# Kernel optimization log

Measured on AMD Instinct MI355X. Metric: run time of the kernel, lower is better.

Reference implementation:

```python
import jax, jax.numpy as jnp
import numpy as np

NUM_EMBEDDINGS = 1024
EMBEDDING_DIM = 64
COMMITMENT_COST = 0.25
DECAY = 0.99
EPS = 1e-5


def setup_inputs() -> dict:
    key = jax.random.key(0)
    k1, k2, k3 = jax.random.split(key, 3)
    z = jax.random.normal(k1, (64, EMBEDDING_DIM, 32, 32), dtype=jnp.float32)
    embedding = jax.random.normal(k2, (NUM_EMBEDDINGS, EMBEDDING_DIM), dtype=jnp.float32)
    cluster_size = jnp.zeros((NUM_EMBEDDINGS,), dtype=jnp.float32)
    ema_w = jax.random.normal(k3, (NUM_EMBEDDINGS, EMBEDDING_DIM), dtype=jnp.float32)
    return {"z": z, "embedding": embedding, "cluster_size": cluster_size, "ema_w": ema_w}


def reference(z, embedding, cluster_size, ema_w):
    B, D, H, W = z.shape
    K = embedding.shape[0]
    # (B, H, W, D) -> (N, D)
    z_flat = jnp.transpose(z, (0, 2, 3, 1)).reshape(-1, D)
    # squared L2 distances to every code: (N, K)
    d = (jnp.sum(z_flat * z_flat, axis=1, keepdims=True)
         + jnp.sum(embedding * embedding, axis=1)
         - 2.0 * z_flat @ embedding.T)
    indices = jnp.argmin(d, axis=1)  # (N,)
    z_q = embedding[indices].reshape(B, H, W, D).transpose(0, 3, 1, 2)

    # EMA codebook update (training branch); no gradients flow here in torch (.data ops)
    zf = jax.lax.stop_gradient(z_flat)
    counts = jax.ops.segment_sum(jnp.ones_like(zf[:, 0]), indices, num_segments=K)
    dw = jax.ops.segment_sum(zf, indices, num_segments=K)  # encodings.T @ z_flat
    new_cluster_size = DECAY * cluster_size + (1.0 - DECAY) * counts
    new_ema_w = DECAY * ema_w + (1.0 - DECAY) * dw
    n = jnp.sum(new_cluster_size)
    cs = (new_cluster_size + EPS) / (n + K * EPS) * n
    new_embedding = new_ema_w / cs[:, None]

    loss = COMMITMENT_COST * jnp.mean((z - jax.lax.stop_gradient(z_q)) ** 2)
    z_q_st = z + jax.lax.stop_gradient(z_q - z)  # straight-through
    return (z_q_st, loss, indices.reshape(B, H, W), new_cluster_size, new_ema_w, new_embedding)
```

## Files before the change

kernel.cpp:

```cpp
#include <hip/hip_runtime.h>
#include <stdint.h>

typedef unsigned short ushort;
typedef __attribute__((ext_vector_type(8)))  short bfrag;
typedef __attribute__((ext_vector_type(16))) float f32x16;

#define D      64
#define K      1024
#define HW     1024
#define NROWS  65536
#define NELEM  (NROWS * D)
#define BAND   0.01f

#define O_ZQ   0
#define O_LOSS 4194304
#define O_IDX  4194305
#define O_NCS  4259841
#define O_EMAW 4260865
#define O_EMB  4326401

#define WB_KEYS   0x000000
#define WB_BUCKET 0x040000
#define WB_EH     0x080000
#define WB_EL     0x0A0000
#define WB_ESQ    0x0C0000
#define WB_OFFS   0x0C1000
#define WB_CURSOR 0x0C2000
#define WB_COUNTS 0x0C3000
#define WB_LOSSN  0x0C4000
#define WB_RLIST  0x0C5000
#define WB_ZH     0x105000
#define WB_END_T1 0x905000

__device__ __forceinline__ unsigned bf16r(float x) {
    unsigned u = __float_as_uint(x);
    return (u + 0x7FFFu + ((u >> 16) & 1u)) >> 16;
}
__device__ __forceinline__ float bf16f(unsigned h) {
    return __uint_as_float(h << 16);
}

__global__ __launch_bounds__(64) void vq_prep_e(
    const float* __restrict__ emb, ushort* __restrict__ eh,
    ushort* __restrict__ el, float* __restrict__ esq)
{
    const int k = blockIdx.x * 64 + threadIdx.x;
    const float* er = emb + (size_t)k * 64;
    float a = 0.f;
    for (int d = 0; d < 64; ++d) {
        float v = er[d];
        a = fmaf(v, v, a);
        unsigned hh = bf16r(v);
        float rem = v - bf16f(hh);
        unsigned ll = bf16r(rem);
        eh[k * 64 + d] = (ushort)hh;
        el[k * 64 + d] = (ushort)ll;
    }
    esq[k] = a;
}

__global__ __launch_bounds__(256, 3) void vq_dist_kernel(
    const float* __restrict__ z, const short* __restrict__ eh_g,
    const short* __restrict__ el_g, const float* __restrict__ esq_g,
    int* __restrict__ keys, unsigned* __restrict__ counts,
    unsigned* __restrict__ rcnt, int* __restrict__ rlist,
    ushort* __restrict__ zh_g, int dump)
{
    __shared__ __align__(16) short zh_lds[128 * 64];
    __shared__ __align__(16) short zl_lds[128 * 64];
    __shared__ __align__(16) short eh_lds[64 * 64];
    __shared__ __align__(16) short el_lds[64 * 64];
    __shared__ float esq_lds[1024];

    const int tid  = threadIdx.x;
    const int lane = tid & 63;
    const int wave = tid >> 6;
    const int col  = lane & 31;
    const int h    = lane >> 5;
    const int n0   = blockIdx.x * 128;
    const int b    = n0 >> 10;
    const int hw0  = n0 & 1023;

    for (int it = 0; it < 4; ++it) {
        int task = it * 256 + tid;
        int row  = task & 127;
        int kq   = task >> 7;
        const float* zp = z + (size_t)b * 65536 + (size_t)(kq * 8) * 1024 + hw0 + row;
        bfrag vh, vl;
#pragma unroll
        for (int m = 0; m < 8; ++m) {
            float v = zp[m * 1024];
            unsigned hh = bf16r(v);
            float rem = v - bf16f(hh);
            vh[m] = (short)hh;
            vl[m] = (short)bf16r(rem);
        }
        int unit = kq ^ (row & 7);
        *(bfrag*)&zh_lds[row * 64 + unit * 8] = vh;
        *(bfrag*)&zl_lds[row * 64 + unit * 8] = vl;
    }
    for (int it = 0; it < 4; ++it) {
        int t = it * 256 + tid;
        esq_lds[t] = esq_g[t];
    }
    __syncthreads();

    const int wrow = wave * 32 + col;
    bfrag zhA[4], zlA[4];
#pragma unroll
    for (int j = 0; j < 4; ++j) {
        int kq = j * 2 + h;
        int unit = kq ^ (wrow & 7);
        zhA[j] = *(const bfrag*)&zh_lds[wrow * 64 + unit * 8];
        zlA[j] = *(const bfrag*)&zl_lds[wrow * 64 + unit * 8];
    }

    if (dump) {
        for (int it = 0; it < 4; ++it) {
            int task = it * 256 + tid;
            int row  = task >> 3;
            int kq   = task & 7;
            int unit = kq ^ (row & 7);
            uint4 v = *(const uint4*)&zh_lds[row * 64 + unit * 8];
            *(uint4*)&zh_g[(size_t)(n0 + row) * 64 + kq * 8] = v;
        }
    }

    float t1s[16], t2s[16];
    unsigned t1c[16];
#pragma unroll
    for (int i = 0; i < 16; ++i) { t1s[i] = INFINITY; t2s[i] = INFINITY; t1c[i] = 0; }

    bfrag pfh[2], pfl[2];
    auto loadE = [&](int cb) {
#pragma unroll
        for (int q = 0; q < 2; ++q) {
            int u = q * 256 + tid;
            int code = u >> 3, m = u & 7;
            pfh[q] = *(const bfrag*)&eh_g[(size_t)(cb + code) * 64 + m * 8];
            pfl[q] = *(const bfrag*)&el_g[(size_t)(cb + code) * 64 + m * 8];
        }
    };
    auto writeE = [&]() {
#pragma unroll
        for (int q = 0; q < 2; ++q) {
            int u = q * 256 + tid;
            int code = u >> 3, m = u & 7;
            int unit = ((code >> 5) * 4 + (m >> 1)) * 64 +
                       ((((m & 1) << 5) | (code & 31)) ^ (m & 7));
            *(bfrag*)&eh_lds[unit * 8] = pfh[q];
            *(bfrag*)&el_lds[unit * 8] = pfl[q];
        }
    };

    loadE(0);
    for (int ch = 0; ch < 16; ++ch) {
        const int cb = ch * 64;
        __syncthreads();
        writeE();
        __syncthreads();
        if (ch < 15) loadE(cb + 64);

#pragma unroll
        for (int t = 0; t < 2; ++t) {
            bfrag ehB[4], elB[4];
#pragma unroll
            for (int j = 0; j < 4; ++j) {
                int m = j * 2 + h;
                int unit = (t * 4 + j) * 64 + (((h << 5) | col) ^ (m & 7));
                ehB[j] = *(const bfrag*)&eh_lds[unit * 8];
                elB[j] = *(const bfrag*)&el_lds[unit * 8];
            }
            f32x16 acc1 = {}, acc2 = {};
#pragma unroll
            for (int j = 0; j < 4; ++j)
                acc1 = __builtin_amdgcn_mfma_f32_32x32x16_bf16(zhA[j], ehB[j], acc1, 0, 0, 0);
#pragma unroll
            for (int j = 0; j < 4; ++j)
                acc2 = __builtin_amdgcn_mfma_f32_32x32x16_bf16(zhA[j], elB[j], acc2, 0, 0, 0);
#pragma unroll
            for (int j = 0; j < 4; ++j)
                acc2 = __builtin_amdgcn_mfma_f32_32x32x16_bf16(zlA[j], ehB[j], acc2, 0, 0, 0);

            const float esqv = esq_lds[cb + t * 32 + col];
            const unsigned ccode = cb + t * 32 + col;
#pragma unroll
            for (int i = 0; i < 16; ++i) {
                float s = fmaf(-2.f, acc1[i], esqv);
                s = fmaf(-2.f, acc2[i], s);
                float mx = fmaxf(s, t1s[i]);
                t2s[i] = fminf(t2s[i], mx);
                bool lt = s < t1s[i];
                t1s[i] = fminf(t1s[i], s);
                t1c[i] = lt ? ccode : t1c[i];
            }
        }
    }

#pragma unroll
    for (int i = 0; i < 16; ++i) {
        float v = t1s[i], w = t2s[i];
        int   c = (int)t1c[i];
#pragma unroll
        for (int m = 1; m < 32; m <<= 1) {
            float ov = __shfl_xor(v, m);
            int   oc = __shfl_xor(c, m);
            float ow = __shfl_xor(w, m);
            float mx = fmaxf(v, ov);
            w = fminf(fminf(w, ow), mx);
            bool take = (ov < v) || (ov == v && oc < c);
            v = take ? ov : v;
            c = take ? oc : c;
        }
        if ((lane & 31) == 0) {
            int row = (i & 3) + ((i >> 2) << 3) + (h << 2);
            int n = n0 + wave * 32 + row;
            keys[n] = c;
            atomicAdd(&counts[c], 1u);
            if (w - v < BAND) {
                unsigned p = atomicAdd(rcnt, 1u);
                rlist[p] = n;
            }
        }
    }
}

__global__ __launch_bounds__(256) void vq_rescore(
    const float* __restrict__ z, const float* __restrict__ emb,
    const float* __restrict__ esq, const unsigned* __restrict__ rcnt,
    const int* __restrict__ rlist, int* __restrict__ keys,
    unsigned* __restrict__ counts)
{
    __shared__ float zrow[64];
    __shared__ float rs[4];
    __shared__ int   rc[4];
    const int tid = threadIdx.x;
    const unsigned cnt = rcnt[0];

    for (unsigned i = blockIdx.x; i < cnt; i += gridDim.x) {
        const int n = rlist[i];
        const int b = n >> 10, hw = n & 1023;
        __syncthreads();
        if (tid < 64) zrow[tid] = z[(size_t)b * 65536 + (size_t)tid * 1024 + hw];
        __syncthreads();

        float best = INFINITY; int bc = 0;
        for (int rep = 0; rep < 4; ++rep) {
            int code = rep * 256 + tid;
            const float4* er = (const float4*)(emb + (size_t)code * 64);
            float a0 = 0.f, a1 = 0.f, a2 = 0.f, a3 = 0.f;
#pragma unroll
            for (int q = 0; q < 16; ++q) {
                float4 e = er[q];
                a0 = fmaf(zrow[q * 4 + 0], e.x, a0);
                a1 = fmaf(zrow[q * 4 + 1], e.y, a1);
                a2 = fmaf(zrow[q * 4 + 2], e.z, a2);
                a3 = fmaf(zrow[q * 4 + 3], e.w, a3);
            }
            float s = fmaf(-2.f, (a0 + a1) + (a2 + a3), esq[code]);
            if (s < best || (s == best && code < bc)) { best = s; bc = code; }
        }
        for (int m = 1; m < 64; m <<= 1) {
            float ov = __shfl_xor(best, m);
            int   oc = __shfl_xor(bc, m);
            bool take = (ov < best) || (ov == best && oc < bc);
            best = take ? ov : best;
            bc   = take ? oc : bc;
        }
        if ((tid & 63) == 0) { rs[tid >> 6] = best; rc[tid >> 6] = bc; }
        __syncthreads();
        if (tid == 0) {
            float fb = rs[0]; int fc = rc[0];
#pragma unroll
            for (int q = 1; q < 4; ++q) {
                bool take = (rs[q] < fb) || (rs[q] == fb && rc[q] < fc);
                fb = take ? rs[q] : fb;
                fc = take ? rc[q] : fc;
            }
            int old = keys[n];
            if (fc != old) {
                atomicAdd(&counts[old], (unsigned)-1);
                atomicAdd(&counts[fc], 1u);
                keys[n] = fc;
            }
        }
    }
}

__global__ __launch_bounds__(1024) void vq_scan_kernel(
    const unsigned* __restrict__ counts, const float* __restrict__ cs,
    unsigned* __restrict__ offs, unsigned* __restrict__ cursor,
    float* __restrict__ out, float* __restrict__ n_val)
{
    __shared__ unsigned wtot[16], wbase[16];
    __shared__ float    fred[16];
    const int k    = threadIdx.x;
    const int lane = k & 63;
    const int w    = k >> 6;

    unsigned c = counts[k];
    unsigned v = c;
#pragma unroll
    for (int off = 1; off < 64; off <<= 1) {
        unsigned t = __shfl_up(v, off);
        if (lane >= off) v += t;
    }
    if (lane == 63) wtot[w] = v;

    float ncs = 0.99f * cs[k] + 0.01f * (float)c;
    out[O_NCS + k] = ncs;
    float s = ncs;
#pragma unroll
    for (int off = 32; off; off >>= 1) s += __shfl_down(s, off);
    if (lane == 0) fred[w] = s;

    __syncthreads();
    if (k == 0) {
        unsigned base = 0;
        float nt = 0.f;
#pragma unroll
        for (int i = 0; i < 16; ++i) {
            wbase[i] = base;
            base += wtot[i];
            nt += fred[i];
        }
        n_val[0] = nt;
    }
    __syncthreads();
    unsigned o = wbase[w] + (v - c);
    offs[k]   = o;
    cursor[k] = o;
}

__global__ __launch_bounds__(256) void vq_epilogue_kernel(
    const float* __restrict__ z, const float* __restrict__ emb,
    const int* __restrict__ keys, float* __restrict__ out,
    unsigned* __restrict__ cursor, int* __restrict__ bucket,
    float* __restrict__ loss_acc)
{
    const int tid = threadIdx.x;
    const int n   = blockIdx.x * 128 + (tid & 127);
    const int h   = tid >> 7;
    const int b   = n >> 10;
    const int hw  = n & 1023;
    const int k   = keys[n];

    const float*  zb  = z   + ((size_t)(b * D + h * 32)) * HW + hw;
    float*        oq  = out + O_ZQ + ((size_t)(b * D + h * 32)) * HW + hw;
    const float4* ek4 = (const float4*)emb + (size_t)k * 16 + h * 8;

    float lacc = 0.f;
#pragma unroll
    for (int i = 0; i < 8; ++i) {
        float4 e = ek4[i];
        float z0 = zb[(i * 4 + 0) * HW];
        float z1 = zb[(i * 4 + 1) * HW];
        float z2 = zb[(i * 4 + 2) * HW];
        float z3 = zb[(i * 4 + 3) * HW];
        oq[(i * 4 + 0) * HW] = z0 + (e.x - z0);
        oq[(i * 4 + 1) * HW] = z1 + (e.y - z1);
        oq[(i * 4 + 2) * HW] = z2 + (e.z - z2);
        oq[(i * 4 + 3) * HW] = z3 + (e.w - z3);
        float d0 = z0 - e.x, d1 = z1 - e.y, d2 = z2 - e.z, d3 = z3 - e.w;
        lacc = fmaf(d0, d0, lacc);
        lacc = fmaf(d1, d1, lacc);
        lacc = fmaf(d2, d2, lacc);
        lacc = fmaf(d3, d3, lacc);
    }

    if (h == 0) {
        out[O_IDX + n] = (float)k;
        unsigned pos = atomicAdd(&cursor[k], 1u);
        bucket[pos]  = n;
    }

    for (int off = 32; off; off >>= 1) lacc += __shfl_down(lacc, off);
    if ((tid & 63) == 0) atomicAdd(loss_acc, lacc);
}

template <int MODE>
__global__ __launch_bounds__(256) void vq_upd_kernel(
    const float* __restrict__ z, const ushort* __restrict__ zh,
    const int* __restrict__ bucket, const unsigned* __restrict__ offs,
    const unsigned* __restrict__ counts, const float* __restrict__ ema_w,
    const float* __restrict__ n_val, const float* __restrict__ loss_acc,
    float* __restrict__ out)
{
    __shared__ float red[4][64];
    const int k   = blockIdx.x;
    const int tid = threadIdx.x;
    const int d   = tid & 63;
    const int q   = tid >> 6;
    const unsigned off = offs[k];
    const unsigned cnt = counts[k];

    auto zload = [&](int r) -> float {
        if (MODE == 1)
            return __uint_as_float((unsigned)zh[(size_t)r * 64 + d] << 16);
        return z[(size_t)(r >> 10) * (D * HW) + (size_t)d * HW + (r & 1023)];
    };

    float acc = 0.f;
    unsigned j = q;
    for (; j + 12 < cnt; j += 16) {
        int r0 = bucket[off + j];
        int r1 = bucket[off + j + 4];
        int r2 = bucket[off + j + 8];
        int r3 = bucket[off + j + 12];
        acc += zload(r0); acc += zload(r1); acc += zload(r2); acc += zload(r3);
    }
    for (; j < cnt; j += 4) acc += zload(bucket[off + j]);

    red[q][d] = acc;
    __syncthreads();
    if (q == 0) {
        float dw = red[0][d] + red[1][d] + red[2][d] + red[3][d];
        float nw = 0.99f * ema_w[k * 64 + d] + 0.01f * dw;
        out[O_EMAW + k * 64 + d] = nw;
        float n   = n_val[0];
        float ncs = out[O_NCS + k];
        float csv = (ncs + 1e-5f) / (n + 1024e-5f) * n;
        out[O_EMB + k * 64 + d] = nw / csv;
    }
    if (k == 0 && tid == 0)
        out[O_LOSS] = 0.25f * loss_acc[0] / (float)NELEM;
}

extern "C" void kernel_launch(void* const* d_in, const int* in_sizes, int n_in,
                              void* d_out, int out_size, void* d_ws, size_t ws_size,
                              hipStream_t stream) {
    const float* z     = (const float*)d_in[0];
    const float* emb   = (const float*)d_in[1];
    const float* cs    = (const float*)d_in[2];
    const float* ema_w = (const float*)d_in[3];
    float* out = (float*)d_out;

    char* W = (char*)d_ws;
    int*      keys   = (int*)(W + WB_KEYS);
    int*      bucket = (int*)(W + WB_BUCKET);
    short*    eh_g   = (short*)(W + WB_EH);
    short*    el_g   = (short*)(W + WB_EL);
    float*    esq    = (float*)(W + WB_ESQ);
    unsigned* offs   = (unsigned*)(W + WB_OFFS);
    unsigned* cursor = (unsigned*)(W + WB_CURSOR);
    unsigned* counts = (unsigned*)(W + WB_COUNTS);
    float*    lossa  = (float*)(W + WB_LOSSN);
    float*    n_val  = lossa + 1;
    unsigned* rcnt   = (unsigned*)(W + WB_LOSSN + 8);
    int*      rlist  = (int*)(W + WB_RLIST);
    ushort*   zh_g   = (ushort*)(W + WB_ZH);

    const int dump = ws_size >= (size_t)WB_END_T1 ? 1 : 0;

    hipMemsetAsync(W + WB_COUNTS, 0, 0x2000, stream);

    vq_prep_e<<<16, 64, 0, stream>>>(emb, (ushort*)eh_g, (ushort*)el_g, esq);
    vq_dist_kernel<<<512, 256, 0, stream>>>(z, eh_g, el_g, esq, keys, counts,
                                            rcnt, rlist, zh_g, dump);
    vq_rescore<<<96, 256, 0, stream>>>(z, emb, esq, rcnt, rlist, keys, counts);
    vq_scan_kernel<<<1, 1024, 0, stream>>>(counts, cs, offs, cursor, out, n_val);
    vq_epilogue_kernel<<<512, 256, 0, stream>>>(z, emb, keys, out, cursor,
                                                bucket, lossa);
    if (dump)
        vq_upd_kernel<1><<<1024, 256, 0, stream>>>(z, zh_g, bucket, offs, counts,
                                                   ema_w, n_val, lossa, out);
    else
        vq_upd_kernel<0><<<1024, 256, 0, stream>>>(z, zh_g, bucket, offs, counts,
                                                   ema_w, n_val, lossa, out);
}
```

Before: 251.1 us.

## Restructure VQ pipeline: double-buffered codebook, fused distance MFMA, scatter z rows via output

The distance kernel now double-buffers codebook chunks in LDS, so each chunk needs one barrier instead of two. It pre-scales z by -2 and seeds the accumulator with the squared code norms, so a single MFMA accumulator gives the distance and the second-best tracking becomes one fmed3. Indices go straight into the output buffer instead of a keys array. The epilogue is split in two: a scatter kernel writes z rows in fp32 row-major into the z_q output region, bucketed by code, and the update kernel reads them contiguously. A final kernel then overwrites that region with the real z_q. The codebook prep kernel is parallelised per element, and the rescore grid is enlarged. Together this removes the bf16 z dump and the indirect bucket gathers, in exchange for an extra full pass over z and using the output region as scratch.

```diff
diff --git a/kernel.cpp b/kernel.cpp
--- a/kernel.cpp
+++ b/kernel.cpp
@@ -19,18 +19,14 @@
 #define O_EMAW 4260865
 #define O_EMB  4326401
 
-#define WB_KEYS   0x000000
-#define WB_BUCKET 0x040000
-#define WB_EH     0x080000
-#define WB_EL     0x0A0000
-#define WB_ESQ    0x0C0000
-#define WB_OFFS   0x0C1000
-#define WB_CURSOR 0x0C2000
-#define WB_COUNTS 0x0C3000
-#define WB_LOSSN  0x0C4000
-#define WB_RLIST  0x0C5000
-#define WB_ZH     0x105000
-#define WB_END_T1 0x905000
+#define WB_EH     0x00000
+#define WB_EL     0x20000
+#define WB_ESQ    0x40000
+#define WB_OFFS   0x41000
+#define WB_CURSOR 0x42000
+#define WB_COUNTS 0x43000
+#define WB_LOSSN  0x44000
+#define WB_RLIST  0x45000
 
 __device__ __forceinline__ unsigned bf16r(float x) {
     unsigned u = __float_as_uint(x);
@@ -44,32 +40,29 @@
     const float* __restrict__ emb, ushort* __restrict__ eh,
     ushort* __restrict__ el, float* __restrict__ esq)
 {
-    const int k = blockIdx.x * 64 + threadIdx.x;
-    const float* er = emb + (size_t)k * 64;
-    float a = 0.f;
-    for (int d = 0; d < 64; ++d) {
-        float v = er[d];
-        a = fmaf(v, v, a);
-        unsigned hh = bf16r(v);
-        float rem = v - bf16f(hh);
-        unsigned ll = bf16r(rem);
-        eh[k * 64 + d] = (ushort)hh;
-        el[k * 64 + d] = (ushort)ll;
-    }
-    esq[k] = a;
-}
-
-__global__ __launch_bounds__(256, 3) void vq_dist_kernel(
+    const int k = blockIdx.x;
+    const int d = threadIdx.x;
+    float v = emb[k * 64 + d];
+    unsigned hh = bf16r(v);
+    float rem = v - bf16f(hh);
+    eh[k * 64 + d] = (ushort)hh;
+    el[k * 64 + d] = (ushort)bf16r(rem);
+    float a = v * v;
+#pragma unroll
+    for (int off = 32; off; off >>= 1) a += __shfl_xor(a, off);
+    if (d == 0) esq[k] = a;
+}
+
+__global__ __launch_bounds__(256, 2) void vq_dist_kernel(
     const float* __restrict__ z, const short* __restrict__ eh_g,
     const short* __restrict__ el_g, const float* __restrict__ esq_g,
-    int* __restrict__ keys, unsigned* __restrict__ counts,
-    unsigned* __restrict__ rcnt, int* __restrict__ rlist,
-    ushort* __restrict__ zh_g, int dump)
+    float* __restrict__ out, unsigned* __restrict__ counts,
+    unsigned* __restrict__ rcnt, int* __restrict__ rlist)
 {
     __shared__ __align__(16) short zh_lds[128 * 64];
     __shared__ __align__(16) short zl_lds[128 * 64];
-    __shared__ __align__(16) short eh_lds[64 * 64];
-    __shared__ __align__(16) short el_lds[64 * 64];
+    __shared__ __align__(16) short eh_lds[2][64 * 64];
+    __shared__ __align__(16) short el_lds[2][64 * 64];
     __shared__ float esq_lds[1024];
 
     const int tid  = threadIdx.x;
@@ -89,9 +82,9 @@
         bfrag vh, vl;
 #pragma unroll
         for (int m = 0; m < 8; ++m) {
-            float v = zp[m * 1024];
-            unsigned hh = bf16r(v);
-            float rem = v - bf16f(hh);
+            float t = -2.0f * zp[m * 1024];
+            unsigned hh = bf16r(t);
+            float rem = t - bf16f(hh);
             vh[m] = (short)hh;
             vl[m] = (short)bf16r(rem);
         }
@@ -103,6 +96,32 @@
         int t = it * 256 + tid;
         esq_lds[t] = esq_g[t];
     }
+
+    bfrag pfh[2], pfl[2];
+    auto loadE = [&](int cb) {
+#pragma unroll
+        for (int q = 0; q < 2; ++q) {
+            int u = q * 256 + tid;
+            int code = u >> 3, m = u & 7;
+            pfh[q] = *(const bfrag*)&eh_g[(size_t)(cb + code) * 64 + m * 8];
+            pfl[q] = *(const bfrag*)&el_g[(size_t)(cb + code) * 64 + m * 8];
+        }
+    };
+    auto writeE = [&](int buf) {
+#pragma unroll
+        for (int q = 0; q < 2; ++q) {
+            int u = q * 256 + tid;
+            int code = u >> 3, m = u & 7;
+            int unit = ((code >> 5) * 4 + (m >> 1)) * 64 +
+                       ((((m & 1) << 5) | (code & 31)) ^ (m & 7));
+            *(bfrag*)&eh_lds[buf][unit * 8] = pfh[q];
+            *(bfrag*)&el_lds[buf][unit * 8] = pfl[q];
+        }
+    };
+
+    loadE(0);
+    writeE(0);
+    loadE(64);
     __syncthreads();
 
     const int wrow = wave * 32 + col;
@@ -115,86 +134,55 @@
         zlA[j] = *(const bfrag*)&zl_lds[wrow * 64 + unit * 8];
     }
 
-    if (dump) {
-        for (int it = 0; it < 4; ++it) {
-            int task = it * 256 + tid;
-            int row  = task >> 3;
-            int kq   = task & 7;
-            int unit = kq ^ (row & 7);
-            uint4 v = *(const uint4*)&zh_lds[row * 64 + unit * 8];
-            *(uint4*)&zh_g[(size_t)(n0 + row) * 64 + kq * 8] = v;
-        }
-    }
-
     float t1s[16], t2s[16];
     unsigned t1c[16];
 #pragma unroll
     for (int i = 0; i < 16; ++i) { t1s[i] = INFINITY; t2s[i] = INFINITY; t1c[i] = 0; }
 
-    bfrag pfh[2], pfl[2];
-    auto loadE = [&](int cb) {
-#pragma unroll
-        for (int q = 0; q < 2; ++q) {
-            int u = q * 256 + tid;
-            int code = u >> 3, m = u & 7;
-            pfh[q] = *(const bfrag*)&eh_g[(size_t)(cb + code) * 64 + m * 8];
-            pfl[q] = *(const bfrag*)&el_g[(size_t)(cb + code) * 64 + m * 8];
-        }
-    };
-    auto writeE = [&]() {
-#pragma unroll
-        for (int q = 0; q < 2; ++q) {
-            int u = q * 256 + tid;
-            int code = u >> 3, m = u & 7;
-            int unit = ((code >> 5) * 4 + (m >> 1)) * 64 +
-                       ((((m & 1) << 5) | (code & 31)) ^ (m & 7));
-            *(bfrag*)&eh_lds[unit * 8] = pfh[q];
-            *(bfrag*)&el_lds[unit * 8] = pfl[q];
-        }
-    };
-
-    loadE(0);
     for (int ch = 0; ch < 16; ++ch) {
-        const int cb = ch * 64;
-        __syncthreads();
-        writeE();
-        __syncthreads();
-        if (ch < 15) loadE(cb + 64);
+        const int cb  = ch * 64;
+        const int buf = ch & 1;
 
 #pragma unroll
         for (int t = 0; t < 2; ++t) {
+            const int ccode = cb + t * 32 + col;
+            const float esqv = esq_lds[ccode];
             bfrag ehB[4], elB[4];
 #pragma unroll
             for (int j = 0; j < 4; ++j) {
                 int m = j * 2 + h;
                 int unit = (t * 4 + j) * 64 + (((h << 5) | col) ^ (m & 7));
-                ehB[j] = *(const bfrag*)&eh_lds[unit * 8];
-                elB[j] = *(const bfrag*)&el_lds[unit * 8];
-            }
-            f32x16 acc1 = {}, acc2 = {};
+                ehB[j] = *(const bfrag*)&eh_lds[buf][unit * 8];
+                elB[j] = *(const bfrag*)&el_lds[buf][unit * 8];
+            }
+            f32x16 acc;
+#pragma unroll
+            for (int i = 0; i < 16; ++i) acc[i] = esqv;
 #pragma unroll
             for (int j = 0; j < 4; ++j)
-                acc1 = __builtin_amdgcn_mfma_f32_32x32x16_bf16(zhA[j], ehB[j], acc1, 0, 0, 0);
+                acc = __builtin_amdgcn_mfma_f32_32x32x16_bf16(zhA[j], ehB[j], acc, 0, 0, 0);
 #pragma unroll
             for (int j = 0; j < 4; ++j)
-                acc2 = __builtin_amdgcn_mfma_f32_32x32x16_bf16(zhA[j], elB[j], acc2, 0, 0, 0);
+                acc = __builtin_amdgcn_mfma_f32_32x32x16_bf16(zhA[j], elB[j], acc, 0, 0, 0);
 #pragma unroll
             for (int j = 0; j < 4; ++j)
-                acc2 = __builtin_amdgcn_mfma_f32_32x32x16_bf16(zlA[j], ehB[j], acc2, 0, 0, 0);
-
-            const float esqv = esq_lds[cb + t * 32 + col];
-            const unsigned ccode = cb + t * 32 + col;
+                acc = __builtin_amdgcn_mfma_f32_32x32x16_bf16(zlA[j], ehB[j], acc, 0, 0, 0);
+
 #pragma unroll
             for (int i = 0; i < 16; ++i) {
-                float s = fmaf(-2.f, acc1[i], esqv);
-                s = fmaf(-2.f, acc2[i], s);
-                float mx = fmaxf(s, t1s[i]);
-                t2s[i] = fminf(t2s[i], mx);
+                float s = acc[i];
+                t2s[i] = __builtin_amdgcn_fmed3f(t1s[i], t2s[i], s);
                 bool lt = s < t1s[i];
                 t1s[i] = fminf(t1s[i], s);
-                t1c[i] = lt ? ccode : t1c[i];
-            }
-        }
+                t1c[i] = lt ? (unsigned)ccode : t1c[i];
+            }
+        }
+
+        if (ch < 15) {
+            writeE(buf ^ 1);
+            if (ch < 14) loadE(cb + 128);
+        }
+        __syncthreads();
     }
 
 #pragma unroll
@@ -215,7 +203,7 @@
         if ((lane & 31) == 0) {
             int row = (i & 3) + ((i >> 2) << 3) + (h << 2);
             int n = n0 + wave * 32 + row;
-            keys[n] = c;
+            out[O_IDX + n] = (float)c;
             atomicAdd(&counts[c], 1u);
             if (w - v < BAND) {
                 unsigned p = atomicAdd(rcnt, 1u);
@@ -228,7 +216,7 @@
 __global__ __launch_bounds__(256) void vq_rescore(
     const float* __restrict__ z, const float* __restrict__ emb,
     const float* __restrict__ esq, const unsigned* __restrict__ rcnt,
-    const int* __restrict__ rlist, int* __restrict__ keys,
+    const int* __restrict__ rlist, float* __restrict__ out,
     unsigned* __restrict__ counts)
 {
     __shared__ float zrow[64];
@@ -277,11 +265,11 @@
                 fb = take ? rs[q] : fb;
                 fc = take ? rc[q] : fc;
             }
-            int old = keys[n];
+            int old = (int)out[O_IDX + n];
             if (fc != old) {
                 atomicAdd(&counts[old], (unsigned)-1);
                 atomicAdd(&counts[fc], 1u);
-                keys[n] = fc;
+                out[O_IDX + n] = (float)fc;
             }
         }
     }
@@ -332,24 +320,97 @@
     cursor[k] = o;
 }
 
-__global__ __launch_bounds__(256) void vq_epilogue_kernel(
+__global__ __launch_bounds__(256) void vq_scatter_kernel(
     const float* __restrict__ z, const float* __restrict__ emb,
-    const int* __restrict__ keys, float* __restrict__ out,
-    unsigned* __restrict__ cursor, int* __restrict__ bucket,
+    float* __restrict__ out, unsigned* __restrict__ cursor,
     float* __restrict__ loss_acc)
+{
+    const int tid = threadIdx.x;
+    const int n   = blockIdx.x * 256 + tid;
+    const int b   = n >> 10;
+    const int hw  = n & 1023;
+    const int k   = (int)out[O_IDX + n];
+
+    const unsigned pos = atomicAdd(&cursor[k], 1u);
+    const float*  zb  = z + (size_t)b * 65536 + hw;
+    const float4* ek4 = (const float4*)emb + (size_t)k * 16;
+    float* dst = out + O_ZQ + (size_t)pos * 64;
+
+    float lacc = 0.f;
+#pragma unroll
+    for (int i = 0; i < 16; ++i) {
+        float4 e = ek4[i];
+        float z0 = zb[(i * 4 + 0) * 1024];
+        float z1 = zb[(i * 4 + 1) * 1024];
+        float z2 = zb[(i * 4 + 2) * 1024];
+        float z3 = zb[(i * 4 + 3) * 1024];
+        *(float4*)&dst[i * 4] = make_float4(z0, z1, z2, z3);
+        float d0 = z0 - e.x, d1 = z1 - e.y, d2 = z2 - e.z, d3 = z3 - e.w;
+        lacc = fmaf(d0, d0, lacc);
+        lacc = fmaf(d1, d1, lacc);
+        lacc = fmaf(d2, d2, lacc);
+        lacc = fmaf(d3, d3, lacc);
+    }
+
+    for (int off = 32; off; off >>= 1) lacc += __shfl_down(lacc, off);
+    if ((tid & 63) == 0) atomicAdd(loss_acc, lacc);
+}
+
+__global__ __launch_bounds__(256) void vq_upd_kernel(
+    const float* __restrict__ zf, const unsigned* __restrict__ offs,
+    const unsigned* __restrict__ counts, const float* __restrict__ ema_w,
+    const float* __restrict__ n_val, const float* __restrict__ loss_acc,
+    float* __restrict__ out)
+{
+    __shared__ float red[4][64];
+    const int k   = blockIdx.x;
+    const int tid = threadIdx.x;
+    const int d   = tid & 63;
+    const int q   = tid >> 6;
+    const unsigned off = offs[k];
+    const unsigned cnt = counts[k];
+
+    float acc = 0.f;
+    unsigned j = q;
+    for (; j + 12 < cnt; j += 16) {
+        float v0 = zf[(size_t)(off + j)      * 64 + d];
+        float v1 = zf[(size_t)(off + j + 4)  * 64 + d];
+        float v2 = zf[(size_t)(off + j + 8)  * 64 + d];
+        float v3 = zf[(size_t)(off + j + 12) * 64 + d];
+        acc += v0; acc += v1; acc += v2; acc += v3;
+    }
+    for (; j < cnt; j += 4) acc += zf[(size_t)(off + j) * 64 + d];
+
+    red[q][d] = acc;
+    __syncthreads();
+    if (q == 0) {
+        float dw = red[0][d] + red[1][d] + red[2][d] + red[3][d];
+        float nw = 0.99f * ema_w[k * 64 + d] + 0.01f * dw;
+        out[O_EMAW + k * 64 + d] = nw;
+        float n   = n_val[0];
+        float ncs = out[O_NCS + k];
+        float csv = (ncs + 1e-5f) / (n + 1024e-5f) * n;
+        out[O_EMB + k * 64 + d] = nw / csv;
+    }
+    if (k == 0 && tid == 0)
+        out[O_LOSS] = 0.25f * loss_acc[0] / (float)NELEM;
+}
+
+__global__ __launch_bounds__(256) void vq_zqwrite_kernel(
+    const float* __restrict__ z, const float* __restrict__ emb,
+    float* __restrict__ out)
 {
     const int tid = threadIdx.x;
     const int n   = blockIdx.x * 128 + (tid & 127);
     const int h   = tid >> 7;
     const int b   = n >> 10;
     const int hw  = n & 1023;
-    const int k   = keys[n];
+    const int k   = (int)out[O_IDX + n];
 
     const float*  zb  = z   + ((size_t)(b * D + h * 32)) * HW + hw;
     float*        oq  = out + O_ZQ + ((size_t)(b * D + h * 32)) * HW + hw;
     const float4* ek4 = (const float4*)emb + (size_t)k * 16 + h * 8;
 
-    float lacc = 0.f;
 #pragma unroll
     for (int i = 0; i < 8; ++i) {
         float4 e = ek4[i];
@@ -361,69 +422,7 @@
         oq[(i * 4 + 1) * HW] = z1 + (e.y - z1);
         oq[(i * 4 + 2) * HW] = z2 + (e.z - z2);
         oq[(i * 4 + 3) * HW] = z3 + (e.w - z3);
-        float d0 = z0 - e.x, d1 = z1 - e.y, d2 = z2 - e.z, d3 = z3 - e.w;
-        lacc = fmaf(d0, d0, lacc);
-        lacc = fmaf(d1, d1, lacc);
-        lacc = fmaf(d2, d2, lacc);
-        lacc = fmaf(d3, d3, lacc);
-    }
-
-    if (h == 0) {
-        out[O_IDX + n] = (float)k;
-        unsigned pos = atomicAdd(&cursor[k], 1u);
-        bucket[pos]  = n;
-    }
-
-    for (int off = 32; off; off >>= 1) lacc += __shfl_down(lacc, off);
-    if ((tid & 63) == 0) atomicAdd(loss_acc, lacc);
-}
-
-template <int MODE>
-__global__ __launch_bounds__(256) void vq_upd_kernel(
-    const float* __restrict__ z, const ushort* __restrict__ zh,
-    const int* __restrict__ bucket, const unsigned* __restrict__ offs,
-    const unsigned* __restrict__ counts, const float* __restrict__ ema_w,
-    const float* __restrict__ n_val, const float* __restrict__ loss_acc,
-    float* __restrict__ out)
-{
-    __shared__ float red[4][64];
-    const int k   = blockIdx.x;
-    const int tid = threadIdx.x;
-    const int d   = tid & 63;
-    const int q   = tid >> 6;
-    const unsigned off = offs[k];
-    const unsigned cnt = counts[k];
-
-    auto zload = [&](int r) -> float {
-        if (MODE == 1)
-            return __uint_as_float((unsigned)zh[(size_t)r * 64 + d] << 16);
-        return z[(size_t)(r >> 10) * (D * HW) + (size_t)d * HW + (r & 1023)];
-    };
-
-    float acc = 0.f;
-    unsigned j = q;
-    for (; j + 12 < cnt; j += 16) {
-        int r0 = bucket[off + j];
-        int r1 = bucket[off + j + 4];
-        int r2 = bucket[off + j + 8];
-        int r3 = bucket[off + j + 12];
-        acc += zload(r0); acc += zload(r1); acc += zload(r2); acc += zload(r3);
-    }
-    for (; j < cnt; j += 4) acc += zload(bucket[off + j]);
-
-    red[q][d] = acc;
-    __syncthreads();
-    if (q == 0) {
-        float dw = red[0][d] + red[1][d] + red[2][d] + red[3][d];
-        float nw = 0.99f * ema_w[k * 64 + d] + 0.01f * dw;
-        out[O_EMAW + k * 64 + d] = nw;
-        float n   = n_val[0];
-        float ncs = out[O_NCS + k];
-        float csv = (ncs + 1e-5f) / (n + 1024e-5f) * n;
-        out[O_EMB + k * 64 + d] = nw / csv;
-    }
-    if (k == 0 && tid == 0)
-        out[O_LOSS] = 0.25f * loss_acc[0] / (float)NELEM;
+    }
 }
 
 extern "C" void kernel_launch(void* const* d_in, const int* in_sizes, int n_in,
@@ -436,8 +435,6 @@
     float* out = (float*)d_out;
 
     char* W = (char*)d_ws;
-    int*      keys   = (int*)(W + WB_KEYS);
-    int*      bucket = (int*)(W + WB_BUCKET);
     short*    eh_g   = (short*)(W + WB_EH);
     short*    el_g   = (short*)(W + WB_EL);
     float*    esq    = (float*)(W + WB_ESQ);
@@ -448,23 +445,16 @@
     float*    n_val  = lossa + 1;
     unsigned* rcnt   = (unsigned*)(W + WB_LOSSN + 8);
     int*      rlist  = (int*)(W + WB_RLIST);
-    ushort*   zh_g   = (ushort*)(W + WB_ZH);
-
-    const int dump = ws_size >= (size_t)WB_END_T1 ? 1 : 0;
 
     hipMemsetAsync(W + WB_COUNTS, 0, 0x2000, stream);
 
-    vq_prep_e<<<16, 64, 0, stream>>>(emb, (ushort*)eh_g, (ushort*)el_g, esq);
-    vq_dist_kernel<<<512, 256, 0, stream>>>(z, eh_g, el_g, esq, keys, counts,
-                                            rcnt, rlist, zh_g, dump);
-    vq_rescore<<<96, 256, 0, stream>>>(z, emb, esq, rcnt, rlist, keys, counts);
+    vq_prep_e<<<1024, 64, 0, stream>>>(emb, (ushort*)eh_g, (ushort*)el_g, esq);
+    vq_dist_kernel<<<512, 256, 0, stream>>>(z, eh_g, el_g, esq, out, counts,
+                                            rcnt, rlist);
+    vq_rescore<<<512, 256, 0, stream>>>(z, emb, esq, rcnt, rlist, out, counts);
     vq_scan_kernel<<<1, 1024, 0, stream>>>(counts, cs, offs, cursor, out, n_val);
-    vq_epilogue_kernel<<<512, 256, 0, stream>>>(z, emb, keys, out, cursor,
-                                                bucket, lossa);
-    if (dump)
-        vq_upd_kernel<1><<<1024, 256, 0, stream>>>(z, zh_g, bucket, offs, counts,
-                                                   ema_w, n_val, lossa, out);
-    else
-        vq_upd_kernel<0><<<1024, 256, 0, stream>>>(z, zh_g, bucket, offs, counts,
-                                                   ema_w, n_val, lossa, out);
-}
+    vq_scatter_kernel<<<256, 256, 0, stream>>>(z, emb, out, cursor, lossa);
+    vq_upd_kernel<<<1024, 256, 0, stream>>>(out + O_ZQ, offs, counts, ema_w,
+                                            n_val, lossa, out);
+    vq_zqwrite_kernel<<<512, 256, 0, stream>>>(z, emb, out);
+}
```

Measured after the change: 219.7 us. -12.5%, faster.
